# Optimization experiments

Hardware: AMD Instinct MI355X
Metric: run time of the kernel (lower is better)

## Reference

```python
import jax, jax.numpy as jnp
import numpy as np

B, S, D, H = 4, 2048, 1024, 16
DK = D // H
EPS = 1e-5


def setup_inputs() -> dict:
    key = jax.random.key(0)
    ks = jax.random.split(key, 9)
    lim = 1.0 / np.sqrt(DK)  # nn.Linear default init range
    def u(k, shape):
        return jax.random.uniform(k, shape, jnp.float32, -lim, lim)
    return {
        "x": jax.random.normal(ks[0], (B, S, D), jnp.float32),
        "Wq": u(ks[1], (H, DK, DK)),
        "bq": u(ks[2], (H, DK)),
        "Wk": u(ks[3], (H, DK, DK)),
        "bk": u(ks[4], (H, DK)),
        "Wv": u(ks[5], (H, DK, DK)),
        "bv": u(ks[6], (H, DK)),
        "gamma": jnp.ones((D,), jnp.float32),
        "beta": jnp.zeros((D,), jnp.float32),
    }


def reference(x, Wq, bq, Wk, bk, Wv, bv, gamma, beta):
    b, s, d = x.shape
    h, dk = Wq.shape[0], Wq.shape[1]
    xh = x.reshape(b, s, h, dk)  # chunk along feature dim -> per-head slices
    # per-head linear projections (heads batched into one einsum)
    Q = jnp.einsum("bshd,hde->bshe", xh, Wq) + bq
    K = jnp.einsum("bshd,hde->bshe", xh, Wk) + bk
    V = jnp.einsum("bshd,hde->bshe", xh, Wv) + bv
    scale = jnp.sqrt(jnp.asarray(dk, x.dtype))
    scores = jnp.einsum("bshe,bthe->bhst", Q, K) / scale  # [B,H,S,S]
    causal = jnp.tril(jnp.ones((s, s), bool))  # apply_mask=True
    scores = jnp.where(causal, scores, -jnp.inf)
    P = jax.nn.softmax(scores, axis=-1)
    O = jnp.einsum("bhst,bthe->bshe", P, V).reshape(b, s, d)  # concat heads
    # dropout is identity in eval mode; residual + LayerNorm
    y = O + x
    mu = jnp.mean(y, axis=-1, keepdims=True)
    var = jnp.mean(jnp.square(y - mu), axis=-1, keepdims=True)
    return (y - mu) * jax.lax.rsqrt(var + EPS) * gamma + beta
```

## Files before the change

kernel.cpp:

```cpp
#include <hip/hip_runtime.h>
#include <hip/hip_bf16.h>

typedef __bf16 bf16_t;
typedef bf16_t bf16x8 __attribute__((ext_vector_type(8)));
typedef bf16_t bf16x4 __attribute__((ext_vector_type(4)));
typedef float f32x4 __attribute__((ext_vector_type(4)));

#define SEQ    2048
#define DHEAD  64
#define DMODEL 1024
#define KVB    64
#define BHN    64
#define LOG2E  1.4426950408889634f

__device__ __forceinline__ f32x4 mfma16(bf16x8 a, bf16x8 b, f32x4 c) {
  return __builtin_amdgcn_mfma_f32_16x16x32_bf16(a, b, c, 0, 0, 0);
}

__device__ __forceinline__ void gload16(void* l, const void* g) {
  __builtin_amdgcn_global_load_lds(
      (const __attribute__((address_space(1))) unsigned int*)g,
      (__attribute__((address_space(3))) unsigned int*)l,
      16, 0, 0);
}

__global__ __launch_bounds__(256) void qkv_kernel(
    const float* __restrict__ x,
    const float* __restrict__ Wq, const float* __restrict__ bq,
    const float* __restrict__ Wk, const float* __restrict__ bk,
    const float* __restrict__ Wv, const float* __restrict__ bv,
    bf16_t* __restrict__ Qw, bf16_t* __restrict__ Kw, bf16_t* __restrict__ VTw) {
  __shared__ __align__(16) char x_lds[256 * 128];
  __shared__ __align__(16) char w_lds[8192];

  const int bh = blockIdx.y;
  const int b = bh >> 4, h = bh & 15;
  const int s0 = blockIdx.x * 256;
  const int t = threadIdx.x;
  const int w = t >> 6, lane = t & 63;
  const int lo = lane & 15, g = lane >> 4;

#pragma unroll
  for (int p = 0; p < 8; ++p) {
    const int row = p * 32 + (t >> 3);
    const int c = t & 7;
    const float* xp = x + ((size_t)(b * SEQ + s0 + row)) * DMODEL + h * DHEAD + c * 8;
    const float4 f0 = *(const float4*)xp;
    const float4 f1 = *(const float4*)(xp + 4);
    bf16x8 v;
    v[0] = (bf16_t)f0.x; v[1] = (bf16_t)f0.y; v[2] = (bf16_t)f0.z; v[3] = (bf16_t)f0.w;
    v[4] = (bf16_t)f1.x; v[5] = (bf16_t)f1.y; v[6] = (bf16_t)f1.z; v[7] = (bf16_t)f1.w;
    *(bf16x8*)(x_lds + row * 128 + ((c * 16) ^ ((row & 7) << 4))) = v;
  }
  __syncthreads();

  for (int wi = 0; wi < 3; ++wi) {
    const float* Wp = (wi == 0) ? Wq : (wi == 1) ? Wk : Wv;
    const float* Bp = (wi == 0) ? bq : (wi == 1) ? bk : bv;
    bf16_t* Op      = (wi == 0) ? Qw : Kw;

    if (wi > 0) __syncthreads();
    {
      const int d = t >> 2, e0 = (t & 3) * 16;
      const float* wp = Wp + (size_t)(h * 64 + d) * 64 + e0;
      const float4 f0 = *(const float4*)(wp);
      const float4 f1 = *(const float4*)(wp + 4);
      const float4 f2 = *(const float4*)(wp + 8);
      const float4 f3 = *(const float4*)(wp + 12);
      float vals[16];
      vals[0] = f0.x; vals[1] = f0.y; vals[2] = f0.z; vals[3] = f0.w;
      vals[4] = f1.x; vals[5] = f1.y; vals[6] = f1.z; vals[7] = f1.w;
      vals[8] = f2.x; vals[9] = f2.y; vals[10] = f2.z; vals[11] = f2.w;
      vals[12] = f3.x; vals[13] = f3.y; vals[14] = f3.z; vals[15] = f3.w;
#pragma unroll
      for (int j = 0; j < 16; ++j) {
        const int e = e0 + j;
        *(bf16_t*)(w_lds + e * 128 + ((2 * d) ^ ((e & 7) << 4))) = (bf16_t)vals[j];
      }
    }
    __syncthreads();

    bf16x8 wf[2][4];
#pragma unroll
    for (int ct = 0; ct < 4; ++ct)
#pragma unroll
      for (int ks = 0; ks < 2; ++ks)
        wf[ks][ct] = *(const bf16x8*)(w_lds + (ct * 16 + lo) * 128 +
                                      ((ks * 64 + g * 16) ^ ((lo & 7) << 4)));
    float4 biasv[4];
    float biass[4];
    if (wi < 2) {
#pragma unroll
      for (int ct = 0; ct < 4; ++ct)
        biasv[ct] = *(const float4*)(Bp + h * 64 + ct * 16 + g * 4);
    } else {
#pragma unroll
      for (int ct = 0; ct < 4; ++ct) biass[ct] = Bp[h * 64 + ct * 16 + lo];
    }

    const float sc = (wi == 0) ? (0.125f * LOG2E) : 1.0f;
#pragma unroll
    for (int it = 0; it < 4; ++it) {
      const int r0 = it * 64 + w * 16;
      bf16x8 xa[2];
#pragma unroll
      for (int ks = 0; ks < 2; ++ks) {
        const int row = r0 + lo;
        xa[ks] = *(const bf16x8*)(x_lds + row * 128 +
                                  ((ks * 64 + g * 16) ^ ((row & 7) << 4)));
      }
      if (wi < 2) {
#pragma unroll
        for (int ct = 0; ct < 4; ++ct) {
          f32x4 a = (f32x4){0.f, 0.f, 0.f, 0.f};
          a = mfma16(wf[0][ct], xa[0], a);
          a = mfma16(wf[1][ct], xa[1], a);
          bf16x4 pk;
#pragma unroll
          for (int r = 0; r < 4; ++r)
            pk[r] = (bf16_t)((a[r] + ((const float*)&biasv[ct])[r]) * sc);
          *(bf16x4*)(Op + ((size_t)bh * SEQ + s0 + r0 + lo) * DHEAD + ct * 16 + g * 4) = pk;
        }
      } else {
#pragma unroll
        for (int ct = 0; ct < 4; ++ct) {
          f32x4 a = (f32x4){0.f, 0.f, 0.f, 0.f};
          a = mfma16(xa[0], wf[0][ct], a);
          a = mfma16(xa[1], wf[1][ct], a);
          bf16x4 pk;
#pragma unroll
          for (int r = 0; r < 4; ++r) pk[r] = (bf16_t)(a[r] + biass[ct]);
          *(bf16x4*)(VTw + ((size_t)bh * DHEAD + ct * 16 + lo) * SEQ + s0 + r0 + g * 4) = pk;
        }
      }
    }
  }
}

__global__ __launch_bounds__(256, 4) void attn_kernel(
    const bf16_t* __restrict__ Qw, const bf16_t* __restrict__ Kw,
    const bf16_t* __restrict__ VTw, float* __restrict__ Out) {
  __shared__ __align__(16) char stage_lds[2][16384];
  __shared__ __align__(16) char p_lds[4][2048];

  const int f = blockIdx.x;
  const int bh = (f & 7) * 8 + ((f >> 3) & 7);
  const int pair = f >> 6;
  const int b = bh >> 4, h = bh & 15;

  const int t = threadIdx.x;
  const int w = t >> 6, lane = t & 63;
  const int lo = lane & 15, g = lane >> 4;
  char* pbase = &p_lds[w][0];

  const int strow = w * 8 + (lane >> 3);
  const int scol = ((lane & 7) * 16) ^ ((lane >> 3) << 4);
  const char* Kbase = (const char*)(Kw + (size_t)bh * SEQ * DHEAD);
  const char* Vbase = (const char*)(VTw + (size_t)bh * DHEAD * SEQ);
  const bf16_t* Qb = Qw + (size_t)bh * SEQ * DHEAD;
  const int swz = (lo & 7) << 4;

  for (int half = 0; half < 2; ++half) {
    const int qt = half ? (31 - pair) : pair;
    const int q0 = qt * 64;
    const int qw0 = q0 + w * 16;
    const int kts = qt + 1;

    bf16x8 qf[2];
    {
      const bf16_t* qp = Qb + (size_t)(qw0 + lo) * DHEAD + g * 8;
      qf[0] = *(const bf16x8*)(qp);
      qf[1] = *(const bf16x8*)(qp + 32);
    }
    float m_run = -1e30f, l_run = 0.f;
    f32x4 oacc[4];
#pragma unroll
    for (int dt = 0; dt < 4; ++dt) oacc[dt] = (f32x4){0.f, 0.f, 0.f, 0.f};

    __syncthreads();
    {
      char* db = &stage_lds[0][0];
#pragma unroll
      for (int p = 0; p < 2; ++p) {
        gload16(db + p * 4096 + w * 1024,
                Kbase + (size_t)(p * 32 + strow) * 128 + scol);
        gload16(db + 8192 + p * 4096 + w * 1024,
                Vbase + (size_t)(p * 32 + strow) * 4096 + scol);
      }
    }
    int cur = 0;
    for (int kt = 0; kt < kts; ++kt) {
      const int kv0 = kt * KVB;
      __syncthreads();
      if (kt + 1 < kts) {
        const int nk = kv0 + KVB;
        char* db = &stage_lds[cur ^ 1][0];
#pragma unroll
        for (int p = 0; p < 2; ++p) {
          gload16(db + p * 4096 + w * 1024,
                  Kbase + (size_t)(nk + p * 32 + strow) * 128 + scol);
          gload16(db + 8192 + p * 4096 + w * 1024,
                  Vbase + (size_t)(p * 32 + strow) * 4096 + (size_t)nk * 2 + scol);
        }
      }
      const char* kb = &stage_lds[cur][0];
      const char* vb = kb + 8192;

      bf16x8 kf[2][4];
#pragma unroll
      for (int ks = 0; ks < 2; ++ks)
#pragma unroll
        for (int ct = 0; ct < 4; ++ct)
          kf[ks][ct] = *(const bf16x8*)(kb + (ct * 16 + lo) * 128 +
                                        ((ks * 64 + g * 16) ^ swz));
      f32x4 sa[4];
      __builtin_amdgcn_s_setprio(1);
#pragma unroll
      for (int ct = 0; ct < 4; ++ct) {
        f32x4 a = (f32x4){0.f, 0.f, 0.f, 0.f};
        a = mfma16(kf[0][ct], qf[0], a);
        a = mfma16(kf[1][ct], qf[1], a);
        sa[ct] = a;
      }
      __builtin_amdgcn_s_setprio(0);

      if (kt == qt) {
        const int q = qw0 + lo;
#pragma unroll
        for (int ct = 0; ct < 4; ++ct)
#pragma unroll
          for (int r = 0; r < 4; ++r) {
            const int kv = kv0 + ct * 16 + g * 4 + r;
            if (kv > q) sa[ct][r] = -1e30f;
          }
      }
      float mt = -1e30f;
#pragma unroll
      for (int ct = 0; ct < 4; ++ct)
        mt = fmaxf(mt, fmaxf(fmaxf(sa[ct][0], sa[ct][1]),
                             fmaxf(sa[ct][2], sa[ct][3])));
      mt = fmaxf(mt, __shfl_xor(mt, 16));
      mt = fmaxf(mt, __shfl_xor(mt, 32));
      if (__any(mt > m_run + 8.f)) {
        const float mn = fmaxf(m_run, mt);
        const float rs = exp2f(m_run - mn);
        l_run *= rs;
        m_run = mn;
#pragma unroll
        for (int r = 0; r < 4; ++r) {
          const float fr = __shfl(rs, g * 4 + r);
#pragma unroll
          for (int dt = 0; dt < 4; ++dt) oacc[dt][r] *= fr;
        }
      }
      float lt = 0.f;
#pragma unroll
      for (int ct = 0; ct < 4; ++ct) {
        bf16x4 pk;
#pragma unroll
        for (int r = 0; r < 4; ++r) {
          const float pv = exp2f(sa[ct][r] - m_run);
          lt += pv;
          pk[r] = (bf16_t)pv;
        }
        *(bf16x4*)(pbase + lo * 128 + ((ct * 32 + g * 8) ^ swz)) = pk;
      }
      lt += __shfl_xor(lt, 16);
      lt += __shfl_xor(lt, 32);
      l_run += lt;

      bf16x8 vf[2][4];
#pragma unroll
      for (int ks = 0; ks < 2; ++ks)
#pragma unroll
        for (int dt = 0; dt < 4; ++dt)
          vf[ks][dt] = *(const bf16x8*)(vb + (dt * 16 + lo) * 128 +
                                        ((ks * 64 + g * 16) ^ swz));
      __builtin_amdgcn_s_setprio(1);
#pragma unroll
      for (int ks = 0; ks < 2; ++ks) {
        const bf16x8 pa = *(const bf16x8*)(pbase + lo * 128 + ((ks * 64 + g * 16) ^ swz));
#pragma unroll
        for (int dt = 0; dt < 4; ++dt)
          oacc[dt] = mfma16(pa, vf[ks][dt], oacc[dt]);
      }
      __builtin_amdgcn_s_setprio(0);
      cur ^= 1;
    }
    const float inv = 1.f / l_run;
#pragma unroll
    for (int r = 0; r < 4; ++r) {
      const float fr = __shfl(inv, g * 4 + r);
      const int srow = qw0 + g * 4 + r;
      float* op = Out + ((size_t)b * SEQ + srow) * DMODEL + h * DHEAD;
#pragma unroll
      for (int dt = 0; dt < 4; ++dt) op[dt * 16 + lo] = oacc[dt][r] * fr;
    }
  }
}

__global__ __launch_bounds__(256) void ln_kernel(
    const float* __restrict__ x, const float* __restrict__ gamma,
    const float* __restrict__ beta, float* __restrict__ out) {
  __shared__ float red[8];
  const int row = blockIdx.x;
  const int t = threadIdx.x;
  float* orow = out + (size_t)row * DMODEL;
  const float* xrow = x + (size_t)row * DMODEL;

  const float4 o = *(const float4*)(orow + t * 4);
  const float4 xv = *(const float4*)(xrow + t * 4);
  float y0 = o.x + xv.x, y1 = o.y + xv.y, y2 = o.z + xv.z, y3 = o.w + xv.w;
  float s = y0 + y1 + y2 + y3;
  float sq = y0 * y0 + y1 * y1 + y2 * y2 + y3 * y3;
#pragma unroll
  for (int m = 1; m < 64; m <<= 1) {
    s += __shfl_xor(s, m);
    sq += __shfl_xor(sq, m);
  }
  const int w = t >> 6;
  if ((t & 63) == 0) { red[w] = s; red[4 + w] = sq; }
  __syncthreads();
  const float S = red[0] + red[1] + red[2] + red[3];
  const float SQ = red[4] + red[5] + red[6] + red[7];
  const float mu = S * (1.f / DMODEL);
  const float var = SQ * (1.f / DMODEL) - mu * mu;
  const float rstd = rsqrtf(var + 1e-5f);
  const float4 gv = *(const float4*)(gamma + t * 4);
  const float4 bv = *(const float4*)(beta + t * 4);
  float4 res;
  res.x = (y0 - mu) * rstd * gv.x + bv.x;
  res.y = (y1 - mu) * rstd * gv.y + bv.y;
  res.z = (y2 - mu) * rstd * gv.z + bv.z;
  res.w = (y3 - mu) * rstd * gv.w + bv.w;
  *(float4*)(orow + t * 4) = res;
}

extern "C" void kernel_launch(void* const* d_in, const int* in_sizes, int n_in,
                              void* d_out, int out_size, void* d_ws, size_t ws_size,
                              hipStream_t stream) {
  const float* x     = (const float*)d_in[0];
  const float* Wq    = (const float*)d_in[1];
  const float* bq    = (const float*)d_in[2];
  const float* Wk    = (const float*)d_in[3];
  const float* bk    = (const float*)d_in[4];
  const float* Wv    = (const float*)d_in[5];
  const float* bv    = (const float*)d_in[6];
  const float* gamma = (const float*)d_in[7];
  const float* beta  = (const float*)d_in[8];
  float* out = (float*)d_out;

  const size_t per = (size_t)BHN * SEQ * DHEAD;
  bf16_t* Qw  = (bf16_t*)d_ws;
  bf16_t* Kw  = Qw + per;
  bf16_t* VTw = Kw + per;

  qkv_kernel<<<dim3(8, 64), 256, 0, stream>>>(x, Wq, bq, Wk, bk, Wv, bv, Qw, Kw, VTw);
  attn_kernel<<<dim3(1024), 256, 0, stream>>>(Qw, Kw, VTw, out);
  ln_kernel<<<dim3(8192), 256, 0, stream>>>(x, gamma, beta, out);
}
```

Measured before the change: 198.9 us.

## Split KV across waves in attention with in-register P and LDS merge

```diff
diff --git a/kernel.cpp b/kernel.cpp
--- a/kernel.cpp
+++ b/kernel.cpp
@@ -5,23 +5,35 @@
 typedef bf16_t bf16x8 __attribute__((ext_vector_type(8)));
 typedef bf16_t bf16x4 __attribute__((ext_vector_type(4)));
 typedef float f32x4 __attribute__((ext_vector_type(4)));
+typedef short short4_ __attribute__((ext_vector_type(4)));
 
 #define SEQ    2048
 #define DHEAD  64
 #define DMODEL 1024
-#define KVB    64
 #define BHN    64
 #define LOG2E  1.4426950408889634f
+#define NEGBIG (-1e30f)
+#define MASKV  (-1e38f)
 
 __device__ __forceinline__ f32x4 mfma16(bf16x8 a, bf16x8 b, f32x4 c) {
   return __builtin_amdgcn_mfma_f32_16x16x32_bf16(a, b, c, 0, 0, 0);
 }
 
-__device__ __forceinline__ void gload16(void* l, const void* g) {
-  __builtin_amdgcn_global_load_lds(
-      (const __attribute__((address_space(1))) unsigned int*)g,
-      (__attribute__((address_space(3))) unsigned int*)l,
-      16, 0, 0);
+__device__ __forceinline__ f32x4 mfma_k16(bf16x4 a, bf16x4 b, f32x4 c) {
+#if defined(__HIP_DEVICE_COMPILE__)
+#if __has_builtin(__builtin_amdgcn_mfma_f32_16x16x16bf16_1k)
+  return __builtin_amdgcn_mfma_f32_16x16x16bf16_1k(
+      __builtin_bit_cast(short4_, a), __builtin_bit_cast(short4_, b), c, 0, 0, 0);
+#else
+  f32x4 d;
+  asm("v_mfma_f32_16x16x16_bf16 %0, %1, %2, %3"
+      : "=v"(d) : "v"(a), "v"(b), "v"(c));
+  return d;
+#endif
+#else
+  (void)a; (void)b;
+  return c;
+#endif
 }
 
 __global__ __launch_bounds__(256) void qkv_kernel(
@@ -31,7 +43,7 @@
     const float* __restrict__ Wv, const float* __restrict__ bv,
     bf16_t* __restrict__ Qw, bf16_t* __restrict__ Kw, bf16_t* __restrict__ VTw) {
   __shared__ __align__(16) char x_lds[256 * 128];
-  __shared__ __align__(16) char w_lds[8192];
+  __shared__ __align__(16) char w_lds[3][8192];
 
   const int bh = blockIdx.y;
   const int b = bh >> 4, h = bh & 15;
@@ -40,6 +52,26 @@
   const int w = t >> 6, lane = t & 63;
   const int lo = lane & 15, g = lane >> 4;
 
+#pragma unroll
+  for (int wi = 0; wi < 3; ++wi) {
+    const float* Wp = (wi == 0) ? Wq : (wi == 1) ? Wk : Wv;
+    const int d = t >> 2, e0 = (t & 3) * 16;
+    const float* wp = Wp + (size_t)(h * 64 + d) * 64 + e0;
+    const float4 f0 = *(const float4*)(wp);
+    const float4 f1 = *(const float4*)(wp + 4);
+    const float4 f2 = *(const float4*)(wp + 8);
+    const float4 f3 = *(const float4*)(wp + 12);
+    float vals[16];
+    vals[0] = f0.x; vals[1] = f0.y; vals[2] = f0.z; vals[3] = f0.w;
+    vals[4] = f1.x; vals[5] = f1.y; vals[6] = f1.z; vals[7] = f1.w;
+    vals[8] = f2.x; vals[9] = f2.y; vals[10] = f2.z; vals[11] = f2.w;
+    vals[12] = f3.x; vals[13] = f3.y; vals[14] = f3.z; vals[15] = f3.w;
+#pragma unroll
+    for (int j = 0; j < 16; ++j) {
+      const int e = e0 + j;
+      *(bf16_t*)(w_lds[wi] + e * 128 + ((2 * d) ^ ((e & 7) << 4))) = (bf16_t)vals[j];
+    }
+  }
 #pragma unroll
   for (int p = 0; p < 8; ++p) {
     const int row = p * 32 + (t >> 3);
@@ -54,38 +86,17 @@
   }
   __syncthreads();
 
+#pragma unroll
   for (int wi = 0; wi < 3; ++wi) {
-    const float* Wp = (wi == 0) ? Wq : (wi == 1) ? Wk : Wv;
     const float* Bp = (wi == 0) ? bq : (wi == 1) ? bk : bv;
     bf16_t* Op      = (wi == 0) ? Qw : Kw;
 
-    if (wi > 0) __syncthreads();
-    {
-      const int d = t >> 2, e0 = (t & 3) * 16;
-      const float* wp = Wp + (size_t)(h * 64 + d) * 64 + e0;
-      const float4 f0 = *(const float4*)(wp);
-      const float4 f1 = *(const float4*)(wp + 4);
-      const float4 f2 = *(const float4*)(wp + 8);
-      const float4 f3 = *(const float4*)(wp + 12);
-      float vals[16];
-      vals[0] = f0.x; vals[1] = f0.y; vals[2] = f0.z; vals[3] = f0.w;
-      vals[4] = f1.x; vals[5] = f1.y; vals[6] = f1.z; vals[7] = f1.w;
-      vals[8] = f2.x; vals[9] = f2.y; vals[10] = f2.z; vals[11] = f2.w;
-      vals[12] = f3.x; vals[13] = f3.y; vals[14] = f3.z; vals[15] = f3.w;
-#pragma unroll
-      for (int j = 0; j < 16; ++j) {
-        const int e = e0 + j;
-        *(bf16_t*)(w_lds + e * 128 + ((2 * d) ^ ((e & 7) << 4))) = (bf16_t)vals[j];
-      }
-    }
-    __syncthreads();
-
     bf16x8 wf[2][4];
 #pragma unroll
     for (int ct = 0; ct < 4; ++ct)
 #pragma unroll
       for (int ks = 0; ks < 2; ++ks)
-        wf[ks][ct] = *(const bf16x8*)(w_lds + (ct * 16 + lo) * 128 +
+        wf[ks][ct] = *(const bf16x8*)(w_lds[wi] + (ct * 16 + lo) * 128 +
                                       ((ks * 64 + g * 16) ^ ((lo & 7) << 4)));
     float4 biasv[4];
     float biass[4];
@@ -137,164 +148,216 @@
   }
 }
 
-__global__ __launch_bounds__(256, 4) void attn_kernel(
+__global__ __launch_bounds__(256) void attn_kernel(
     const bf16_t* __restrict__ Qw, const bf16_t* __restrict__ Kw,
     const bf16_t* __restrict__ VTw, float* __restrict__ Out) {
-  __shared__ __align__(16) char stage_lds[2][16384];
-  __shared__ __align__(16) char p_lds[4][2048];
+  __shared__ __align__(16) float o_lds[2][4096];
+  __shared__ float ml_m[4][64];
+  __shared__ float ml_l[4][64];
 
   const int f = blockIdx.x;
-  const int bh = (f & 7) * 8 + ((f >> 3) & 7);
-  const int pair = f >> 6;
+  const int idx = f >> 3;
+  const int bh = (f & 7) * 8 + (idx >> 5);
+  const int qt = 31 - (idx & 31);
+  const int q0 = qt * 64;
+  const int kts = qt + 1;
   const int b = bh >> 4, h = bh & 15;
 
   const int t = threadIdx.x;
   const int w = t >> 6, lane = t & 63;
   const int lo = lane & 15, g = lane >> 4;
-  char* pbase = &p_lds[w][0];
-
-  const int strow = w * 8 + (lane >> 3);
-  const int scol = ((lane & 7) * 16) ^ ((lane >> 3) << 4);
-  const char* Kbase = (const char*)(Kw + (size_t)bh * SEQ * DHEAD);
-  const char* Vbase = (const char*)(VTw + (size_t)bh * DHEAD * SEQ);
+
   const bf16_t* Qb = Qw + (size_t)bh * SEQ * DHEAD;
-  const int swz = (lo & 7) << 4;
-
-  for (int half = 0; half < 2; ++half) {
-    const int qt = half ? (31 - pair) : pair;
-    const int q0 = qt * 64;
-    const int qw0 = q0 + w * 16;
-    const int kts = qt + 1;
-
-    bf16x8 qf[2];
-    {
-      const bf16_t* qp = Qb + (size_t)(qw0 + lo) * DHEAD + g * 8;
-      qf[0] = *(const bf16x8*)(qp);
-      qf[1] = *(const bf16x8*)(qp + 32);
-    }
-    float m_run = -1e30f, l_run = 0.f;
-    f32x4 oacc[4];
-#pragma unroll
-    for (int dt = 0; dt < 4; ++dt) oacc[dt] = (f32x4){0.f, 0.f, 0.f, 0.f};
-
-    __syncthreads();
-    {
-      char* db = &stage_lds[0][0];
-#pragma unroll
-      for (int p = 0; p < 2; ++p) {
-        gload16(db + p * 4096 + w * 1024,
-                Kbase + (size_t)(p * 32 + strow) * 128 + scol);
-        gload16(db + 8192 + p * 4096 + w * 1024,
-                Vbase + (size_t)(p * 32 + strow) * 4096 + scol);
-      }
-    }
-    int cur = 0;
-    for (int kt = 0; kt < kts; ++kt) {
-      const int kv0 = kt * KVB;
-      __syncthreads();
-      if (kt + 1 < kts) {
-        const int nk = kv0 + KVB;
-        char* db = &stage_lds[cur ^ 1][0];
-#pragma unroll
-        for (int p = 0; p < 2; ++p) {
-          gload16(db + p * 4096 + w * 1024,
-                  Kbase + (size_t)(nk + p * 32 + strow) * 128 + scol);
-          gload16(db + 8192 + p * 4096 + w * 1024,
-                  Vbase + (size_t)(p * 32 + strow) * 4096 + (size_t)nk * 2 + scol);
-        }
-      }
-      const char* kb = &stage_lds[cur][0];
-      const char* vb = kb + 8192;
-
-      bf16x8 kf[2][4];
-#pragma unroll
-      for (int ks = 0; ks < 2; ++ks)
-#pragma unroll
-        for (int ct = 0; ct < 4; ++ct)
-          kf[ks][ct] = *(const bf16x8*)(kb + (ct * 16 + lo) * 128 +
-                                        ((ks * 64 + g * 16) ^ swz));
-      f32x4 sa[4];
-      __builtin_amdgcn_s_setprio(1);
-#pragma unroll
-      for (int ct = 0; ct < 4; ++ct) {
-        f32x4 a = (f32x4){0.f, 0.f, 0.f, 0.f};
-        a = mfma16(kf[0][ct], qf[0], a);
-        a = mfma16(kf[1][ct], qf[1], a);
-        sa[ct] = a;
-      }
-      __builtin_amdgcn_s_setprio(0);
-
-      if (kt == qt) {
-        const int q = qw0 + lo;
-#pragma unroll
-        for (int ct = 0; ct < 4; ++ct)
-#pragma unroll
-          for (int r = 0; r < 4; ++r) {
-            const int kv = kv0 + ct * 16 + g * 4 + r;
-            if (kv > q) sa[ct][r] = -1e30f;
-          }
-      }
-      float mt = -1e30f;
+  const bf16_t* Kb = Kw + (size_t)bh * SEQ * DHEAD;
+  const bf16_t* Vb = VTw + (size_t)bh * DHEAD * SEQ;
+
+  bf16x8 qf[4][2];
+#pragma unroll
+  for (int ct = 0; ct < 4; ++ct) {
+    const bf16_t* qp = Qb + (size_t)(q0 + ct * 16 + lo) * DHEAD + g * 8;
+    qf[ct][0] = *(const bf16x8*)(qp);
+    qf[ct][1] = *(const bf16x8*)(qp + 32);
+  }
+
+  f32x4 oacc[4][4];
+  float m[4], l[4];
+#pragma unroll
+  for (int ct = 0; ct < 4; ++ct) {
+    m[ct] = NEGBIG;
+    l[ct] = 0.f;
+#pragma unroll
+    for (int dt = 0; dt < 4; ++dt) oacc[ct][dt] = (f32x4){0.f, 0.f, 0.f, 0.f};
+  }
+
+  const int kvw = w * 16;
+  bf16x8 kc0 = *(const bf16x8*)(Kb + (size_t)(kvw + lo) * DHEAD + g * 8);
+  bf16x8 kc1 = *(const bf16x8*)(Kb + (size_t)(kvw + lo) * DHEAD + 32 + g * 8);
+  bf16x4 vc0 = *(const bf16x4*)(Vb + (size_t)(0 * 16 + lo) * SEQ + kvw + g * 4);
+  bf16x4 vc1 = *(const bf16x4*)(Vb + (size_t)(1 * 16 + lo) * SEQ + kvw + g * 4);
+  bf16x4 vc2 = *(const bf16x4*)(Vb + (size_t)(2 * 16 + lo) * SEQ + kvw + g * 4);
+  bf16x4 vc3 = *(const bf16x4*)(Vb + (size_t)(3 * 16 + lo) * SEQ + kvw + g * 4);
+
+  for (int kt = 0; kt < kts; ++kt) {
+    f32x4 sa[4];
+    __builtin_amdgcn_s_setprio(1);
+#pragma unroll
+    for (int ct = 0; ct < 4; ++ct) {
+      f32x4 a = (f32x4){0.f, 0.f, 0.f, 0.f};
+      a = mfma16(kc0, qf[ct][0], a);
+      a = mfma16(kc1, qf[ct][1], a);
+      sa[ct] = a;
+    }
+    __builtin_amdgcn_s_setprio(0);
+
+    bf16x8 kn0, kn1;
+    bf16x4 vn0, vn1, vn2, vn3;
+    const bool more = (kt + 1 < kts);
+    if (more) {
+      const int nb = (kt + 1) * 64 + kvw;
+      kn0 = *(const bf16x8*)(Kb + (size_t)(nb + lo) * DHEAD + g * 8);
+      kn1 = *(const bf16x8*)(Kb + (size_t)(nb + lo) * DHEAD + 32 + g * 8);
+      vn0 = *(const bf16x4*)(Vb + (size_t)(0 * 16 + lo) * SEQ + nb + g * 4);
+      vn1 = *(const bf16x4*)(Vb + (size_t)(1 * 16 + lo) * SEQ + nb + g * 4);
+      vn2 = *(const bf16x4*)(Vb + (size_t)(2 * 16 + lo) * SEQ + nb + g * 4);
+      vn3 = *(const bf16x4*)(Vb + (size_t)(3 * 16 + lo) * SEQ + nb + g * 4);
+    }
+
+    if (kt == qt) {
 #pragma unroll
       for (int ct = 0; ct < 4; ++ct)
-        mt = fmaxf(mt, fmaxf(fmaxf(sa[ct][0], sa[ct][1]),
-                             fmaxf(sa[ct][2], sa[ct][3])));
+#pragma unroll
+        for (int r = 0; r < 4; ++r)
+          if (kvw + g * 4 + r > ct * 16 + lo) sa[ct][r] = MASKV;
+    }
+
+    bf16x4 pa[4];
+#pragma unroll
+    for (int ct = 0; ct < 4; ++ct) {
+      float mt = fmaxf(fmaxf(sa[ct][0], sa[ct][1]), fmaxf(sa[ct][2], sa[ct][3]));
       mt = fmaxf(mt, __shfl_xor(mt, 16));
       mt = fmaxf(mt, __shfl_xor(mt, 32));
-      if (__any(mt > m_run + 8.f)) {
-        const float mn = fmaxf(m_run, mt);
-        const float rs = exp2f(m_run - mn);
-        l_run *= rs;
-        m_run = mn;
+      if (__any(mt > m[ct] + 8.f)) {
+        const float mn = fmaxf(m[ct], mt);
+        const float rs = exp2f(m[ct] - mn);
+        l[ct] *= rs;
+        m[ct] = mn;
 #pragma unroll
         for (int r = 0; r < 4; ++r) {
           const float fr = __shfl(rs, g * 4 + r);
 #pragma unroll
-          for (int dt = 0; dt < 4; ++dt) oacc[dt][r] *= fr;
+          for (int dt = 0; dt < 4; ++dt) oacc[ct][dt][r] *= fr;
         }
       }
-      float lt = 0.f;
+      bf16x4 pk;
+#pragma unroll
+      for (int r = 0; r < 4; ++r) {
+        const float pv = exp2f(sa[ct][r] - m[ct]);
+        l[ct] += pv;
+        pk[r] = (bf16_t)pv;
+      }
+      pa[ct] = pk;
+    }
+
+    __builtin_amdgcn_s_setprio(1);
+#pragma unroll
+    for (int ct = 0; ct < 4; ++ct) {
+      oacc[ct][0] = mfma_k16(pa[ct], vc0, oacc[ct][0]);
+      oacc[ct][1] = mfma_k16(pa[ct], vc1, oacc[ct][1]);
+      oacc[ct][2] = mfma_k16(pa[ct], vc2, oacc[ct][2]);
+      oacc[ct][3] = mfma_k16(pa[ct], vc3, oacc[ct][3]);
+    }
+    __builtin_amdgcn_s_setprio(0);
+
+    if (more) {
+      kc0 = kn0; kc1 = kn1;
+      vc0 = vn0; vc1 = vn1; vc2 = vn2; vc3 = vn3;
+    }
+  }
+
+#pragma unroll
+  for (int ct = 0; ct < 4; ++ct) {
+    l[ct] += __shfl_xor(l[ct], 16);
+    l[ct] += __shfl_xor(l[ct], 32);
+  }
+  if (g == 0) {
+#pragma unroll
+    for (int ct = 0; ct < 4; ++ct) {
+      ml_m[w][ct * 16 + lo] = m[ct];
+      ml_l[w][ct * 16 + lo] = l[ct];
+    }
+  }
+  if (w & 1) {
+    float* ob = o_lds[w >> 1];
+#pragma unroll
+    for (int ct = 0; ct < 4; ++ct)
+#pragma unroll
+      for (int dt = 0; dt < 4; ++dt)
+        *(f32x4*)(ob + (ct * 4 + dt) * 256 + lane * 4) = oacc[ct][dt];
+  }
+  __syncthreads();
+  if (!(w & 1)) {
+    const int ps = w + 1;
+    float* ob = o_lds[w >> 1];
+#pragma unroll
+    for (int ct = 0; ct < 4; ++ct) {
+      const float ma = m[ct];
+      const float pm = ml_m[ps][ct * 16 + lo];
+      const float pl = ml_l[ps][ct * 16 + lo];
+      float far[4], fbr[4];
+#pragma unroll
+      for (int r = 0; r < 4; ++r) {
+        const float ma_r = __shfl(ma, g * 4 + r);
+        const float pm_r = ml_m[ps][ct * 16 + g * 4 + r];
+        const float mn_r = fmaxf(ma_r, pm_r);
+        far[r] = exp2f(ma_r - mn_r);
+        fbr[r] = exp2f(pm_r - mn_r);
+      }
+#pragma unroll
+      for (int dt = 0; dt < 4; ++dt) {
+        const f32x4 obv = *(const f32x4*)(ob + (ct * 4 + dt) * 256 + lane * 4);
+#pragma unroll
+        for (int r = 0; r < 4; ++r)
+          oacc[ct][dt][r] = oacc[ct][dt][r] * far[r] + obv[r] * fbr[r];
+      }
+      const float mn = fmaxf(ma, pm);
+      l[ct] = l[ct] * exp2f(ma - mn) + pl * exp2f(pm - mn);
+      m[ct] = mn;
+    }
+    if (g == 0) {
 #pragma unroll
       for (int ct = 0; ct < 4; ++ct) {
-        bf16x4 pk;
-#pragma unroll
-        for (int r = 0; r < 4; ++r) {
-          const float pv = exp2f(sa[ct][r] - m_run);
-          lt += pv;
-          pk[r] = (bf16_t)pv;
-        }
-        *(bf16x4*)(pbase + lo * 128 + ((ct * 32 + g * 8) ^ swz)) = pk;
-      }
-      lt += __shfl_xor(lt, 16);
-      lt += __shfl_xor(lt, 32);
-      l_run += lt;
-
-      bf16x8 vf[2][4];
-#pragma unroll
-      for (int ks = 0; ks < 2; ++ks)
-#pragma unroll
-        for (int dt = 0; dt < 4; ++dt)
-          vf[ks][dt] = *(const bf16x8*)(vb + (dt * 16 + lo) * 128 +
-                                        ((ks * 64 + g * 16) ^ swz));
-      __builtin_amdgcn_s_setprio(1);
-#pragma unroll
-      for (int ks = 0; ks < 2; ++ks) {
-        const bf16x8 pa = *(const bf16x8*)(pbase + lo * 128 + ((ks * 64 + g * 16) ^ swz));
-#pragma unroll
-        for (int dt = 0; dt < 4; ++dt)
-          oacc[dt] = mfma16(pa, vf[ks][dt], oacc[dt]);
-      }
-      __builtin_amdgcn_s_setprio(0);
-      cur ^= 1;
-    }
-    const float inv = 1.f / l_run;
+        ml_m[w][ct * 16 + lo] = m[ct];
+        ml_l[w][ct * 16 + lo] = l[ct];
+      }
+    }
+#pragma unroll
+    for (int ct = 0; ct < 4; ++ct)
+#pragma unroll
+      for (int dt = 0; dt < 4; ++dt)
+        *(f32x4*)(ob + (ct * 4 + dt) * 256 + lane * 4) = oacc[ct][dt];
+  }
+  __syncthreads();
+#pragma unroll
+  for (int ct = 0; ct < 4; ++ct) {
+    float far[4], fbr[4], inv[4];
 #pragma unroll
     for (int r = 0; r < 4; ++r) {
-      const float fr = __shfl(inv, g * 4 + r);
-      const int srow = qw0 + g * 4 + r;
-      float* op = Out + ((size_t)b * SEQ + srow) * DMODEL + h * DHEAD;
-#pragma unroll
-      for (int dt = 0; dt < 4; ++dt) op[dt * 16 + lo] = oacc[dt][r] * fr;
+      const float ma_r = ml_m[0][ct * 16 + g * 4 + r];
+      const float mb_r = ml_m[2][ct * 16 + g * 4 + r];
+      const float mn_r = fmaxf(ma_r, mb_r);
+      far[r] = exp2f(ma_r - mn_r);
+      fbr[r] = exp2f(mb_r - mn_r);
+      const float la_r = ml_l[0][ct * 16 + g * 4 + r];
+      const float lb_r = ml_l[2][ct * 16 + g * 4 + r];
+      inv[r] = 1.0f / (la_r * far[r] + lb_r * fbr[r]);
+    }
+    const f32x4 Oa = *(const f32x4*)(o_lds[0] + (ct * 4 + w) * 256 + lane * 4);
+    const f32x4 Ob = *(const f32x4*)(o_lds[1] + (ct * 4 + w) * 256 + lane * 4);
+#pragma unroll
+    for (int r = 0; r < 4; ++r) {
+      const float val = (Oa[r] * far[r] + Ob[r] * fbr[r]) * inv[r];
+      Out[((size_t)(b * SEQ + q0 + ct * 16 + g * 4 + r)) * DMODEL +
+          h * DHEAD + w * 16 + lo] = val;
     }
   }
 }
@@ -356,6 +419,6 @@
   bf16_t* VTw = Kw + per;
 
   qkv_kernel<<<dim3(8, 64), 256, 0, stream>>>(x, Wq, bq, Wk, bk, Wv, bv, Qw, Kw, VTw);
-  attn_kernel<<<dim3(1024), 256, 0, stream>>>(Qw, Kw, VTw, out);
+  attn_kernel<<<dim3(2048), 256, 0, stream>>>(Qw, Kw, VTw, out);
   ln_kernel<<<dim3(8192), 256, 0, stream>>>(x, gamma, beta, out);
 }
```

Measured after the change: 316.2 us. +59.0%, slower.
